# Performance work log

Measured on AMD Instinct MI355X. Metric: run time of the kernel, lower is better.

The kernel has to match this reference:

```python
import jax, jax.numpy as jnp
import numpy as np

D_IN = 784
D = 768          # hidden_dim
R = 8            # num_rels
L = 3            # num_layers
B = 64           # graphs in batch
N = 32768        # total nodes
E = 262144       # total edges


def _layer_norm(x, g, b, eps=1e-5):
    m = x.mean(-1, keepdims=True)
    v = x.var(-1, keepdims=True)
    return (x - m) / jnp.sqrt(v + eps) * g + b


def setup_inputs() -> dict:
    key = jax.random.key(0)
    ks = jax.random.split(key, 24)
    s = 0.02
    inp = {
        "type_vec": jax.random.normal(ks[0], (N, 16), jnp.float32),
        "code_vec": jax.random.normal(ks[1], (N, D), jnp.float32),
        # input_proj: Linear(784,768) + LayerNorm(768)
        "W_in": jax.random.normal(ks[2], (D_IN, D), jnp.float32) * s,
        "b_in": jnp.zeros((D,), jnp.float32),
        "ln_in_g": jnp.ones((D,), jnp.float32),
        "ln_in_b": jnp.zeros((D,), jnp.float32),
        # RGCN layers (basis regularizer, num_bases=num_rels -> per-relation W)
        "W_rel": jax.random.normal(ks[3], (L, R, D, D), jnp.float32) * s,
        "W_loop": jax.random.normal(ks[4], (L, D, D), jnp.float32) * s,
        "rgcn_bias": jnp.zeros((L, D), jnp.float32),
        "ln_g": jnp.ones((L, D), jnp.float32),
        "ln_b": jnp.zeros((L, D), jnp.float32),
        # global attention pooling gate MLP: 768 -> 384 -> 1
        "Wg1": jax.random.normal(ks[5], (D, D // 2), jnp.float32) * s,
        "bg1": jnp.zeros((D // 2,), jnp.float32),
        "Wg2": jax.random.normal(ks[6], (D // 2, 1), jnp.float32) * s,
        "bg2": jnp.zeros((1,), jnp.float32),
        # classifier: 768 -> 512 (+LN) -> 2
        "Wc1": jax.random.normal(ks[7], (D, 512), jnp.float32) * s,
        "bc1": jnp.zeros((512,), jnp.float32),
        "ln_c_g": jnp.ones((512,), jnp.float32),
        "ln_c_b": jnp.zeros((512,), jnp.float32),
        "Wc2": jax.random.normal(ks[8], (512, 2), jnp.float32) * s,
        "bc2": jnp.zeros((2,), jnp.float32),
        # graph structure
        "src": jax.random.randint(ks[9], (E,), 0, N, jnp.int64),
        "dst": jax.random.randint(ks[10], (E,), 0, N, jnp.int64),
        "edge_type": jax.random.randint(ks[11], (E,), 0, R, jnp.int64),
        "node_graph": jnp.sort(jax.random.randint(ks[12], (N,), 0, B, jnp.int64)),
        "num_graphs": B,
    }
    return inp


def reference(type_vec, code_vec, W_in, b_in, ln_in_g, ln_in_b,
              W_rel, W_loop, rgcn_bias, ln_g, ln_b,
              Wg1, bg1, Wg2, bg2, Wc1, bc1, ln_c_g, ln_c_b, Wc2, bc2,
              src, dst, edge_type, node_graph, num_graphs):
    # input projection
    h = jnp.concatenate([type_vec, code_vec], axis=-1)           # [N, 784]
    h = jax.nn.gelu(_layer_norm(h @ W_in + b_in, ln_in_g, ln_in_b), approximate=False)
    n_nodes = h.shape[0]
    n_layers, n_rels = W_rel.shape[0], W_rel.shape[1]

    for l in range(n_layers):
        agg = jnp.zeros_like(h)
        for r in range(n_rels):
            # relation-specific transform, then gather->mask->scatter-add
            msg = (h @ W_rel[l, r])[src] * (edge_type == r).astype(h.dtype)[:, None]  # [E, D]
            agg = agg + jax.ops.segment_sum(msg, dst, num_segments=n_nodes)
        h_new = agg + rgcn_bias[l] + h @ W_loop[l]               # DGL: agg + bias + self-loop
        h = jax.nn.gelu(_layer_norm(h_new, ln_g[l], ln_b[l]), approximate=False)

    # global attention pooling (segment softmax over nodes of each graph)
    gate = (jax.nn.gelu(h @ Wg1 + bg1, approximate=False) @ Wg2 + bg2)[:, 0]  # [N]
    gmax = jax.ops.segment_max(gate, node_graph, num_segments=num_graphs)
    e = jnp.exp(gate - gmax[node_graph])
    denom = jax.ops.segment_sum(e, node_graph, num_segments=num_graphs)
    w = e / denom[node_graph]
    graph_repr = jax.ops.segment_sum(w[:, None] * h, node_graph, num_segments=num_graphs)  # [B, D]

    # classifier head
    z = jax.nn.gelu(_layer_norm(graph_repr @ Wc1 + bc1, ln_c_g, ln_c_b), approximate=False)
    logits = z @ Wc2 + bc2
    return jax.nn.log_softmax(logits, axis=-1)
```

## Files before the change

kernel.cpp:

```cpp
#include <hip/hip_runtime.h>
#include <hip/hip_bf16.h>

typedef __hip_bfloat16 bf16;
typedef __attribute__((ext_vector_type(8))) __bf16 bf16x8;
typedef __attribute__((ext_vector_type(4))) float f32x4;

#define N_NODES 32768
#define N_EDGES 262144
#define DIM 768
#define NGR 64
#define KIN 800
#define KSTACK 6912
#define NKEY (N_NODES * 8)

#define GLOBAL_AS __attribute__((address_space(1)))
#define LDS_AS __attribute__((address_space(3)))

__device__ __forceinline__ float gelu_f(float x) {
    return 0.5f * x * (1.0f + erff(x * 0.70710678118654752f));
}
__device__ __forceinline__ float bfu(unsigned short v) {
    union { unsigned u; float f; } x; x.u = (unsigned)v << 16; return x.f;
}
__device__ __forceinline__ unsigned short fbf(float f) {
    bf16 t = __float2bfloat16(f); return *(unsigned short*)&t;
}

__global__ __launch_bounds__(256)
void tcast_k(const float* __restrict__ in, bf16* __restrict__ out, int I, int O,
             int Ipad, int ostride) {
    __shared__ float t[32][33];
    const int i0 = blockIdx.x * 32, o0 = blockIdx.y * 32;
    const int tx = threadIdx.x & 31, ty = threadIdx.x >> 5;
#pragma unroll
    for (int q = 0; q < 4; ++q) {
        int i = i0 + ty + q * 8, o = o0 + tx;
        t[ty + q * 8][tx] = (i < I) ? in[(size_t)i * O + o] : 0.0f;
    }
    __syncthreads();
#pragma unroll
    for (int q = 0; q < 4; ++q) {
        int o = o0 + ty + q * 8, i = i0 + tx;
        if (i < Ipad) out[(size_t)o * ostride + i] = __float2bfloat16(t[tx][ty + q * 8]);
    }
}

__global__ __launch_bounds__(256)
void wprep_l_k(const float* __restrict__ Wrel_l, const float* __restrict__ Wloop_l,
               bf16* __restrict__ WstL) {
    __shared__ float t[32][33];
    const int q = blockIdx.z;
    const float* in = (q < 8) ? Wrel_l + (size_t)q * DIM * DIM : Wloop_l;
    bf16* out = WstL + (q < 8 ? (q + 1) * DIM : 0);
    const int i0 = blockIdx.x * 32, o0 = blockIdx.y * 32;
    const int tx = threadIdx.x & 31, ty = threadIdx.x >> 5;
#pragma unroll
    for (int qq = 0; qq < 4; ++qq)
        t[ty + qq * 8][tx] = in[(size_t)(i0 + ty + qq * 8) * DIM + o0 + tx];
    __syncthreads();
#pragma unroll
    for (int qq = 0; qq < 4; ++qq)
        out[(size_t)(o0 + ty + qq * 8) * KSTACK + i0 + tx] =
            __float2bfloat16(t[tx][ty + qq * 8]);
}

__global__ __launch_bounds__(256)
void concat_k(const float* __restrict__ tv, const float* __restrict__ cv, bf16* __restrict__ X) {
    const int n = blockIdx.x;
    for (int c = threadIdx.x; c < KIN; c += 256) {
        float v = 0.0f;
        if (c < 16) v = tv[(size_t)n * 16 + c];
        else if (c < 784) v = cv[(size_t)n * DIM + (c - 16)];
        X[(size_t)n * KIN + c] = __float2bfloat16(v);
    }
}

__global__ __launch_bounds__(256)
void hist2_k(const int* __restrict__ dst, const int* __restrict__ et, int* __restrict__ cur) {
    int e = blockIdx.x * 256 + threadIdx.x;
    if (e < N_EDGES) atomicAdd(&cur[dst[e] * 8 + et[e]], 1);
}

__global__ __launch_bounds__(1024)
void scan2_k(int* __restrict__ cur, int* __restrict__ rp) {
    __shared__ int part[1024];
    const int t = threadIdx.x;
    const int base_i = t * 256;
    int s = 0;
    for (int i = 0; i < 256; ++i) s += cur[base_i + i];
    part[t] = s; __syncthreads();
    for (int st = 1; st < 1024; st <<= 1) {
        int v = (t >= st) ? part[t - st] : 0;
        __syncthreads();
        part[t] += v;
        __syncthreads();
    }
    int run = part[t] - s;
    for (int i = 0; i < 256; ++i) {
        int d = cur[base_i + i];
        rp[base_i + i] = run; cur[base_i + i] = run;
        run += d;
    }
    if (t == 1023) rp[NKEY] = run;
}

__global__ __launch_bounds__(256)
void place2_k(const int* __restrict__ src, const int* __restrict__ dst,
              const int* __restrict__ et, int* __restrict__ cur,
              int* __restrict__ eidx) {
    int e = blockIdx.x * 256 + threadIdx.x;
    if (e >= N_EDGES) return;
    int pos = atomicAdd(&cur[dst[e] * 8 + et[e]], 1);
    eidx[pos] = (et[e] << 16) | src[e];
}

template <int NC>
__global__ __launch_bounds__(256)
void gather8(const bf16* __restrict__ h, const int* __restrict__ rp2,
             const int* __restrict__ eidx, bf16* __restrict__ AGG,
             int rbase, int ostride, int colbase) {
    const int wave = threadIdx.x >> 6, lane = threadIdx.x & 63;
    const int n = blockIdx.x * 4 + wave;
    const int c0 = 4 * lane;
    unsigned short* outrow = (unsigned short*)&AGG[(size_t)n * ostride + colbase];
    const int* bp = &rp2[n * 8 + rbase];
    for (int sel = 0; sel < NC; ++sel) {
        const int s = bp[sel], e = bp[sel + 1];
        float f[12];
#pragma unroll
        for (int j = 0; j < 12; ++j) f[j] = 0.f;
        for (int t = s; t < e; ++t) {
            const int srcn = eidx[t] & 0xffff;
            const unsigned short* hs = (const unsigned short*)&h[(size_t)srcn * DIM];
#pragma unroll
            for (int j = 0; j < 3; ++j) {
                ushort4 u = *(const ushort4*)&hs[c0 + j * 256];
                f[4 * j + 0] += bfu(u.x); f[4 * j + 1] += bfu(u.y);
                f[4 * j + 2] += bfu(u.z); f[4 * j + 3] += bfu(u.w);
            }
        }
#pragma unroll
        for (int j = 0; j < 3; ++j) {
            ushort4 o;
            o.x = fbf(f[4 * j + 0]); o.y = fbf(f[4 * j + 1]);
            o.z = fbf(f[4 * j + 2]); o.w = fbf(f[4 * j + 3]);
            *(ushort4*)&outrow[sel * DIM + c0 + j * 256] = o;
        }
    }
}

template <int MODE>
__global__ __launch_bounds__(512, 2)
void gemm384(const bf16* __restrict__ A1, int S1, int K1,
             const bf16* __restrict__ A2, int S2,
             const bf16* __restrict__ BT, int ldb,
             bf16* __restrict__ OUT, int Nn, int Ktot, int nbx) {
    __shared__ __align__(16) unsigned short lA[3][256 * 32];
    __shared__ __align__(16) unsigned short lB[3][384 * 32];
    const int nblk = gridDim.x, qx = nblk >> 3, bid = blockIdx.x;
    const int wgid = (bid & 7) * qx + (bid >> 3);
    const int bx = wgid % nbx, by = wgid / nbx;
    const int bn = bx * 384, bm = by * 256;
    const int tid = threadIdx.x;
    const int wave = tid >> 6, lane = tid & 63;
    const int wr = wave >> 1, wc = wave & 1;
    const int l15 = lane & 15, lg = lane >> 4;
    const int swz = (lg ^ ((l15 >> 1) & 3)) * 8;

    f32x4 acc[4][12] = {};
    const int nkt = Ktot >> 5;

    auto stage = [&](int t, int buf) {
        const int k0 = t * 32;
        const bf16* Ab; int koff, stA;
        if (k0 < K1) { Ab = A1; koff = k0; stA = S1; }
        else         { Ab = A2; koff = k0 - K1; stA = S2; }
#pragma unroll
        for (int u = 0; u < 2; ++u) {
            const int c = u * 512 + tid;
            const int r = c >> 2, s = c & 3;
            const int sc = (s ^ ((r >> 1) & 3)) * 8;
            const bf16* ga = Ab + (size_t)(bm + r) * stA + koff + sc;
            __builtin_amdgcn_global_load_lds((const GLOBAL_AS void*)ga,
                (LDS_AS void*)&lA[buf][(u * 512 + wave * 64) * 8], 16, 0, 0);
        }
#pragma unroll
        for (int u = 0; u < 3; ++u) {
            const int c = u * 512 + tid;
            const int r = c >> 2, s = c & 3;
            const int sc = (s ^ ((r >> 1) & 3)) * 8;
            const bf16* gb = BT + (size_t)(bn + r) * ldb + k0 + sc;
            __builtin_amdgcn_global_load_lds((const GLOBAL_AS void*)gb,
                (LDS_AS void*)&lB[buf][(u * 512 + wave * 64) * 8], 16, 0, 0);
        }
    };

    stage(0, 0);
    if (nkt > 1) stage(1, 1);

    int rb = 0;
    for (int t = 0; t < nkt; ++t) {
        if (t + 2 < nkt) {
            int sb = rb + 2; if (sb >= 3) sb -= 3;
            stage(t + 2, sb);
            asm volatile("s_waitcnt vmcnt(10)" ::: "memory");
        } else if (t + 1 < nkt) {
            asm volatile("s_waitcnt vmcnt(5)" ::: "memory");
        } else {
            asm volatile("s_waitcnt vmcnt(0)" ::: "memory");
        }
        __builtin_amdgcn_s_barrier();
        __builtin_amdgcn_sched_barrier(0);

        bf16x8 af[4];
#pragma unroll
        for (int mi = 0; mi < 4; ++mi) {
            const int r = wr * 64 + mi * 16 + l15;
            af[mi] = *reinterpret_cast<const bf16x8*>(&lA[rb][r * 32 + swz]);
        }
        __builtin_amdgcn_s_setprio(1);
#pragma unroll
        for (int ni = 0; ni < 12; ++ni) {
            const int r = wc * 192 + ni * 16 + l15;
            bf16x8 bq = *reinterpret_cast<const bf16x8*>(&lB[rb][r * 32 + swz]);
#pragma unroll
            for (int mi = 0; mi < 4; ++mi)
                acc[mi][ni] = __builtin_amdgcn_mfma_f32_16x16x32_bf16(af[mi], bq, acc[mi][ni], 0, 0, 0);
        }
        __builtin_amdgcn_s_setprio(0);
        __builtin_amdgcn_sched_barrier(0);
        __builtin_amdgcn_s_barrier();

        rb = (rb == 2) ? 0 : rb + 1;
    }

    unsigned short* O = (unsigned short*)OUT;
#pragma unroll
    for (int mi = 0; mi < 4; ++mi)
#pragma unroll
        for (int ni = 0; ni < 12; ++ni) {
            const int r0 = bm + wr * 64 + mi * 16 + lg * 4;
            const int c0 = bn + wc * 192 + ni * 16 + l15;
#pragma unroll
            for (int i = 0; i < 4; ++i) {
                size_t idx = (size_t)(r0 + i) * Nn + c0;
                float v = acc[mi][ni][i];
                if (MODE == 1) v += bfu(O[idx]);
                O[idx] = fbf(v);
            }
        }
}

__global__ __launch_bounds__(256)
void ln_gelu_k(const bf16* __restrict__ ACCb, const float* __restrict__ bias,
               const float* __restrict__ g, const float* __restrict__ b,
               bf16* __restrict__ hout) {
    const int wave = threadIdx.x >> 6, lane = threadIdx.x & 63;
    const int n = blockIdx.x * 4 + wave;
    const unsigned short* Ab = (const unsigned short*)ACCb;
    float x[12];
    float s = 0.f, ss = 0.f;
#pragma unroll
    for (int j = 0; j < 12; ++j) {
        int c = lane + j * 64;
        x[j] = bfu(Ab[(size_t)n * DIM + c]) + bias[c];
        s += x[j]; ss += x[j] * x[j];
    }
#pragma unroll
    for (int m = 1; m < 64; m <<= 1) { s += __shfl_xor(s, m, 64); ss += __shfl_xor(ss, m, 64); }
    const float mean = s * (1.f / DIM);
    const float var = ss * (1.f / DIM) - mean * mean;
    const float rstd = rsqrtf(var + 1e-5f);
#pragma unroll
    for (int j = 0; j < 12; ++j) {
        int c = lane + j * 64;
        float y = (x[j] - mean) * rstd * g[c] + b[c];
        hout[(size_t)n * DIM + c] = __float2bfloat16(gelu_f(y));
    }
}

__global__ __launch_bounds__(256)
void gate_k(const bf16* __restrict__ G1, const float* __restrict__ bg1,
            const float* __restrict__ Wg2, const float* __restrict__ bg2,
            float* __restrict__ gate) {
    const int wave = threadIdx.x >> 6, lane = threadIdx.x & 63;
    const int n = blockIdx.x * 4 + wave;
    const unsigned short* G = (const unsigned short*)G1;
    float acc = 0.f;
#pragma unroll
    for (int j = 0; j < 6; ++j) {
        int c = lane + j * 64;
        float xv = bfu(G[(size_t)n * 384 + c]) + bg1[c];
        acc += gelu_f(xv) * Wg2[c];
    }
#pragma unroll
    for (int m = 1; m < 64; m <<= 1) acc += __shfl_xor(acc, m, 64);
    if (lane == 0) gate[n] = acc + bg2[0];
}

__device__ __forceinline__ int lower_bound_ng(const int* ng, int key) {
    int lo = 0, hi = N_NODES;
    while (lo < hi) { int mid = (lo + hi) >> 1; if (ng[mid] < key) lo = mid + 1; else hi = mid; }
    return lo;
}

__global__ __launch_bounds__(256)
void seg_stats_k(const float* __restrict__ gate, const int* __restrict__ ng,
                 float* __restrict__ gmax, float* __restrict__ gden) {
    __shared__ float red[256];
    const int b = blockIdx.x, t = threadIdx.x;
    const int start = lower_bound_ng(ng, b), end = lower_bound_ng(ng, b + 1);
    float m = -1e30f;
    for (int n = start + t; n < end; n += 256) m = fmaxf(m, gate[n]);
    red[t] = m; __syncthreads();
    for (int s = 128; s > 0; s >>= 1) { if (t < s) red[t] = fmaxf(red[t], red[t + s]); __syncthreads(); }
    const float gm = red[0]; __syncthreads();
    float ssum = 0.f;
    for (int n = start + t; n < end; n += 256) ssum += expf(gate[n] - gm);
    red[t] = ssum; __syncthreads();
    for (int s = 128; s > 0; s >>= 1) { if (t < s) red[t] += red[t + s]; __syncthreads(); }
    if (t == 0) { gmax[b] = gm; gden[b] = fmaxf(red[0], 1e-30f); }
}

__global__ __launch_bounds__(768)
void pool_k(const bf16* __restrict__ h, const float* __restrict__ gate,
            const int* __restrict__ ng, const float* __restrict__ gmax,
            const float* __restrict__ gden, float* __restrict__ grep) {
    const int b = blockIdx.x, c = threadIdx.x;
    const int start = lower_bound_ng(ng, b), end = lower_bound_ng(ng, b + 1);
    const float gm = gmax[b], inv = 1.0f / gden[b];
    const unsigned short* hv = (const unsigned short*)h;
    float a0 = 0.f, a1 = 0.f;
    int n = start;
    for (; n + 1 < end; n += 2) {
        float w0 = expf(gate[n] - gm) * inv;
        float w1 = expf(gate[n + 1] - gm) * inv;
        a0 += w0 * bfu(hv[(size_t)n * DIM + c]);
        a1 += w1 * bfu(hv[(size_t)(n + 1) * DIM + c]);
    }
    if (n < end) a0 += expf(gate[n] - gm) * inv * bfu(hv[(size_t)n * DIM + c]);
    grep[(size_t)b * DIM + c] = a0 + a1;
}

__global__ __launch_bounds__(512)
void cls_k(const float* __restrict__ grep, const float* __restrict__ Wc1,
           const float* __restrict__ bc1, const float* __restrict__ lng,
           const float* __restrict__ lnb, const float* __restrict__ Wc2,
           const float* __restrict__ bc2, float* __restrict__ out) {
    __shared__ float gr[DIM];
    __shared__ float red[512];
    const int b = blockIdx.x, j = threadIdx.x;
    for (int c = j; c < DIM; c += 512) gr[c] = grep[(size_t)b * DIM + c];
    __syncthreads();
    float a = bc1[j];
#pragma unroll 4
    for (int k = 0; k < DIM; ++k) a = fmaf(gr[k], Wc1[(size_t)k * 512 + j], a);
    red[j] = a; __syncthreads();
    for (int s = 256; s > 0; s >>= 1) { if (j < s) red[j] += red[j + s]; __syncthreads(); }
    const float mean = red[0] * (1.f / 512.f);
    __syncthreads();
    red[j] = (a - mean) * (a - mean); __syncthreads();
    for (int s = 256; s > 0; s >>= 1) { if (j < s) red[j] += red[j + s]; __syncthreads(); }
    const float rstd = rsqrtf(red[0] * (1.f / 512.f) + 1e-5f);
    __syncthreads();
    const float z = gelu_f((a - mean) * rstd * lng[j] + lnb[j]);
    red[j] = z * Wc2[2 * j + 0]; __syncthreads();
    for (int s = 256; s > 0; s >>= 1) { if (j < s) red[j] += red[j + s]; __syncthreads(); }
    const float l0 = red[0] + bc2[0];
    __syncthreads();
    red[j] = z * Wc2[2 * j + 1]; __syncthreads();
    for (int s = 256; s > 0; s >>= 1) { if (j < s) red[j] += red[j + s]; __syncthreads(); }
    if (j == 0) {
        const float l1 = red[0] + bc2[1];
        const float mx = fmaxf(l0, l1);
        const float lse = mx + logf(expf(l0 - mx) + expf(l1 - mx));
        out[2 * b + 0] = l0 - lse;
        out[2 * b + 1] = l1 - lse;
    }
}

extern "C" void kernel_launch(void* const* d_in, const int* in_sizes, int n_in,
                              void* d_out, int out_size, void* d_ws, size_t ws_size,
                              hipStream_t stream) {
    const float* type_vec = (const float*)d_in[0];
    const float* code_vec = (const float*)d_in[1];
    const float* W_in     = (const float*)d_in[2];
    const float* b_in     = (const float*)d_in[3];
    const float* ln_in_g  = (const float*)d_in[4];
    const float* ln_in_b  = (const float*)d_in[5];
    const float* W_rel    = (const float*)d_in[6];
    const float* W_loop   = (const float*)d_in[7];
    const float* rgcn_bias= (const float*)d_in[8];
    const float* ln_g     = (const float*)d_in[9];
    const float* ln_b     = (const float*)d_in[10];
    const float* Wg1      = (const float*)d_in[11];
    const float* bg1      = (const float*)d_in[12];
    const float* Wg2      = (const float*)d_in[13];
    const float* bg2      = (const float*)d_in[14];
    const float* Wc1      = (const float*)d_in[15];
    const float* bc1      = (const float*)d_in[16];
    const float* ln_c_g   = (const float*)d_in[17];
    const float* ln_c_b   = (const float*)d_in[18];
    const float* Wc2      = (const float*)d_in[19];
    const float* bc2      = (const float*)d_in[20];
    const int* src        = (const int*)d_in[21];
    const int* dst        = (const int*)d_in[22];
    const int* etype      = (const int*)d_in[23];
    const int* node_graph = (const int*)d_in[24];

    char* ws = (char*)d_ws;

    auto lay = [&](int nc, bool doAssign,
                   bf16*& h_bf, bf16*& ACCb, bf16*& WstL, int*& rp2, int*& cur2,
                   int*& eidx, float*& gate, float*& gmax, float*& gden,
                   float*& grep, bf16*& AGG) -> size_t {
        size_t off = 0;
        auto alloc = [&](size_t sz) { size_t r = off; off = (off + sz + 255) & ~(size_t)255; return r; };
        size_t oH   = alloc((size_t)N_NODES * DIM * 2);
        size_t oAC  = alloc((size_t)N_NODES * DIM * 2);
        size_t oWL  = alloc((size_t)DIM * KSTACK * 2);
        size_t oRP  = alloc((size_t)(NKEY + 1) * 4);
        size_t oCU  = alloc((size_t)NKEY * 4);
        size_t oEI  = alloc((size_t)N_EDGES * 4);
        size_t oGA  = alloc((size_t)N_NODES * 4);
        size_t oGM  = alloc(256);
        size_t oGD  = alloc(256);
        size_t oGR  = alloc((size_t)NGR * DIM * 4);
        size_t oAG  = alloc((size_t)N_NODES * nc * DIM * 2);
        if (doAssign) {
            h_bf = (bf16*)(ws + oH);   ACCb = (bf16*)(ws + oAC);
            WstL = (bf16*)(ws + oWL);  rp2  = (int*)(ws + oRP);
            cur2 = (int*)(ws + oCU);   eidx = (int*)(ws + oEI);
            gate = (float*)(ws + oGA); gmax = (float*)(ws + oGM);
            gden = (float*)(ws + oGD); grep = (float*)(ws + oGR);
            AGG  = (bf16*)(ws + oAG);
        }
        return off;
    };

    bf16 *h_bf, *ACCb, *WstL, *AGG; int *rp2, *cur2, *eidx;
    float *gate, *gmax, *gden, *grep;
    bf16 *d0=nullptr,*d1=nullptr,*d2=nullptr,*d3=nullptr; int *d4=nullptr,*d5=nullptr,*d6=nullptr;
    float *d7=nullptr,*d8=nullptr,*d9=nullptr,*d10=nullptr;
    const bool big = ws_size >= lay(8, false, d0,d1,d2,d4,d5,d6,d7,d8,d9,d10,d3);
    const int nc = big ? 8 : 4;
    lay(nc, true, h_bf, ACCb, WstL, rp2, cur2, eidx, gate, gmax, gden, grep, AGG);

    bf16* Xbf  = AGG;
    bf16* WinT = (bf16*)((char*)AGG + (size_t)N_NODES * KIN * 2);
    bf16* G1   = AGG;

    const int AGW = nc * DIM;

    tcast_k<<<dim3(25, 24), 256, 0, stream>>>(W_in, WinT, 784, DIM, KIN, KIN);
    concat_k<<<N_NODES, 256, 0, stream>>>(type_vec, code_vec, Xbf);
    gemm384<0><<<256, 512, 0, stream>>>(Xbf, KIN, KIN, Xbf, KIN, WinT, KIN, ACCb, DIM, KIN, 2);
    ln_gelu_k<<<N_NODES / 4, 256, 0, stream>>>(ACCb, b_in, ln_in_g, ln_in_b, h_bf);

    hipMemsetAsync(cur2, 0, (size_t)NKEY * 4, stream);
    hist2_k<<<N_EDGES / 256, 256, 0, stream>>>(dst, etype, cur2);
    scan2_k<<<1, 1024, 0, stream>>>(cur2, rp2);
    place2_k<<<N_EDGES / 256, 256, 0, stream>>>(src, dst, etype, cur2, eidx);

    for (int l = 0; l < 3; ++l) {
        wprep_l_k<<<dim3(24, 24, 9), 256, 0, stream>>>(
            W_rel + (size_t)l * 8 * DIM * DIM, W_loop + (size_t)l * DIM * DIM, WstL);
        if (nc == 8) {
            gather8<8><<<N_NODES / 4, 256, 0, stream>>>(h_bf, rp2, eidx, AGG, 0, AGW, 0);
            gemm384<0><<<256, 512, 0, stream>>>(
                h_bf, DIM, DIM, AGG, AGW, WstL, KSTACK, ACCb, DIM, KSTACK, 2);
        } else {
            gather8<4><<<N_NODES / 4, 256, 0, stream>>>(h_bf, rp2, eidx, AGG, 0, AGW, 0);
            gemm384<0><<<256, 512, 0, stream>>>(
                h_bf, DIM, DIM, AGG, AGW, WstL, KSTACK, ACCb, DIM, DIM + 4 * DIM, 2);
            gather8<4><<<N_NODES / 4, 256, 0, stream>>>(h_bf, rp2, eidx, AGG, 4, AGW, 0);
            gemm384<1><<<256, 512, 0, stream>>>(
                AGG, AGW, AGW, AGG, AGW, WstL + (size_t)DIM * 5, KSTACK, ACCb, DIM, 4 * DIM, 2);
        }
        ln_gelu_k<<<N_NODES / 4, 256, 0, stream>>>(ACCb, rgcn_bias + l * DIM, ln_g + l * DIM,
                                                   ln_b + l * DIM, h_bf);
    }

    bf16* Wg1T = (bf16*)((char*)AGG + 60 * 1024 * 1024);
    tcast_k<<<dim3(24, 12), 256, 0, stream>>>(Wg1, Wg1T, DIM, 384, DIM, DIM);
    gemm384<0><<<128, 512, 0, stream>>>(h_bf, DIM, DIM, h_bf, DIM, Wg1T, DIM, G1, 384, DIM, 1);
    gate_k<<<N_NODES / 4, 256, 0, stream>>>(G1, bg1, Wg2, bg2, gate);
    seg_stats_k<<<NGR, 256, 0, stream>>>(gate, node_graph, gmax, gden);
    pool_k<<<NGR, 768, 0, stream>>>(h_bf, gate, node_graph, gmax, gden, grep);

    cls_k<<<NGR, 512, 0, stream>>>(grep, Wc1, bc1, ln_c_g, ln_c_b, Wc2, bc2, (float*)d_out);
}
```

Baseline: 2.453 ms.

## Fuse LayerNorm+GELU into full-row GEMM epilogue and single-pass relation gather

Adds a GEMM kernel whose tiles span all 768 output columns. Bias, LayerNorm and GELU can then run in the epilogue, with row statistics reduced through shuffles and LDS. This removes the separate ln_gelu pass and the round trip of the fp32/bf16 accumulator buffer for the input projection and every RGCN layer. It also replaces the per-relation gather loop with one pass over each node's edges that accumulates into eight register sets chosen by relation. The cost is very high register pressure (4x12 MFMA accumulators plus 96 gather accumulators), which risks spills or lower occupancy.

```diff
diff --git a/kernel.cpp b/kernel.cpp
--- a/kernel.cpp
+++ b/kernel.cpp
@@ -114,6 +114,46 @@
     eidx[pos] = (et[e] << 16) | src[e];
 }
 
+__global__ __launch_bounds__(256)
+void gather1p(const bf16* __restrict__ h, const int* __restrict__ rp2,
+              const int* __restrict__ eidx, bf16* __restrict__ AGG, int ostride) {
+    const int wave = threadIdx.x >> 6, lane = threadIdx.x & 63;
+    const int n = blockIdx.x * 4 + wave;
+    const int c0 = 4 * lane;
+    const int start = rp2[n * 8], end = rp2[n * 8 + 8];
+    float f0[12] = {}, f1[12] = {}, f2[12] = {}, f3[12] = {};
+    float f4[12] = {}, f5[12] = {}, f6[12] = {}, f7[12] = {};
+    for (int t = start; t < end; ++t) {
+        const int pk = eidx[t];
+        const int sel = pk >> 16;
+        const unsigned short* hs = (const unsigned short*)&h[(size_t)(pk & 0xffff) * DIM];
+        ushort4 u0 = *(const ushort4*)&hs[c0];
+        ushort4 u1 = *(const ushort4*)&hs[c0 + 256];
+        ushort4 u2 = *(const ushort4*)&hs[c0 + 512];
+#define ADDE(F) { F[0]+=bfu(u0.x); F[1]+=bfu(u0.y); F[2]+=bfu(u0.z); F[3]+=bfu(u0.w); \
+                  F[4]+=bfu(u1.x); F[5]+=bfu(u1.y); F[6]+=bfu(u1.z); F[7]+=bfu(u1.w); \
+                  F[8]+=bfu(u2.x); F[9]+=bfu(u2.y); F[10]+=bfu(u2.z); F[11]+=bfu(u2.w); }
+        switch (sel) {
+            case 0: ADDE(f0) break;
+            case 1: ADDE(f1) break;
+            case 2: ADDE(f2) break;
+            case 3: ADDE(f3) break;
+            case 4: ADDE(f4) break;
+            case 5: ADDE(f5) break;
+            case 6: ADDE(f6) break;
+            default: ADDE(f7) break;
+        }
+#undef ADDE
+    }
+    unsigned short* outrow = (unsigned short*)&AGG[(size_t)n * ostride];
+#define STE(F, S) _Pragma("unroll") for (int j = 0; j < 3; ++j) { ushort4 o; \
+        o.x = fbf(F[4*j+0]); o.y = fbf(F[4*j+1]); o.z = fbf(F[4*j+2]); o.w = fbf(F[4*j+3]); \
+        *(ushort4*)&outrow[(S) * DIM + c0 + j * 256] = o; }
+    STE(f0, 0) STE(f1, 1) STE(f2, 2) STE(f3, 3)
+    STE(f4, 4) STE(f5, 5) STE(f6, 6) STE(f7, 7)
+#undef STE
+}
+
 template <int NC>
 __global__ __launch_bounds__(256)
 void gather8(const bf16* __restrict__ h, const int* __restrict__ rp2,
@@ -147,6 +187,137 @@
             *(ushort4*)&outrow[sel * DIM + c0 + j * 256] = o;
         }
     }
+}
+
+__global__ __launch_bounds__(512, 2)
+void gemm_ln(const bf16* __restrict__ A1, int S1, int K1,
+             const bf16* __restrict__ A2, int S2,
+             const bf16* __restrict__ BT, int ldb,
+             const float* __restrict__ bias, const float* __restrict__ g,
+             const float* __restrict__ b, bf16* __restrict__ OUT, int Ktot) {
+    __shared__ __align__(16) unsigned short lA[2][128 * 32];
+    __shared__ __align__(16) unsigned short lB[2][768 * 32];
+    __shared__ float lred[128][8];
+    const int nblk = gridDim.x, qx = nblk >> 3, bid = blockIdx.x;
+    const int wgid = (bid & 7) * qx + (bid >> 3);
+    const int bm = wgid * 128;
+    const int tid = threadIdx.x;
+    const int wave = tid >> 6, lane = tid & 63;
+    const int wr = wave >> 2, wc = wave & 3;
+    const int l15 = lane & 15, lg = lane >> 4;
+    const int swz = (lg ^ ((l15 >> 1) & 3)) * 8;
+
+    f32x4 acc[4][12] = {};
+    const int nkt = Ktot >> 5;
+
+    auto stage = [&](int t, int buf) {
+        const int k0 = t * 32;
+        const bf16* Ab; int koff, stA;
+        if (k0 < K1) { Ab = A1; koff = k0; stA = S1; }
+        else         { Ab = A2; koff = k0 - K1; stA = S2; }
+        {
+            const int r = tid >> 2, s = tid & 3;
+            const int sc = (s ^ ((r >> 1) & 3)) * 8;
+            const bf16* ga = Ab + (size_t)(bm + r) * stA + koff + sc;
+            __builtin_amdgcn_global_load_lds((const GLOBAL_AS void*)ga,
+                (LDS_AS void*)&lA[buf][(wave * 64) * 8], 16, 0, 0);
+        }
+#pragma unroll
+        for (int u = 0; u < 6; ++u) {
+            const int c = u * 512 + tid;
+            const int r = c >> 2, s = c & 3;
+            const int sc = (s ^ ((r >> 1) & 3)) * 8;
+            const bf16* gb = BT + (size_t)r * ldb + k0 + sc;
+            __builtin_amdgcn_global_load_lds((const GLOBAL_AS void*)gb,
+                (LDS_AS void*)&lB[buf][((u * 8 + wave) * 64) * 8], 16, 0, 0);
+        }
+    };
+
+    stage(0, 0);
+
+    for (int t = 0; t < nkt; ++t) {
+        const int rb = t & 1;
+        if (t + 1 < nkt) {
+            stage(t + 1, rb ^ 1);
+            asm volatile("s_waitcnt vmcnt(7)" ::: "memory");
+        } else {
+            asm volatile("s_waitcnt vmcnt(0)" ::: "memory");
+        }
+        __builtin_amdgcn_s_barrier();
+        __builtin_amdgcn_sched_barrier(0);
+
+        bf16x8 af[4];
+#pragma unroll
+        for (int mi = 0; mi < 4; ++mi) {
+            const int r = wr * 64 + mi * 16 + l15;
+            af[mi] = *reinterpret_cast<const bf16x8*>(&lA[rb][r * 32 + swz]);
+        }
+        __builtin_amdgcn_s_setprio(1);
+#pragma unroll
+        for (int ni = 0; ni < 12; ++ni) {
+            const int r = wc * 192 + ni * 16 + l15;
+            bf16x8 bq = *reinterpret_cast<const bf16x8*>(&lB[rb][r * 32 + swz]);
+#pragma unroll
+            for (int mi = 0; mi < 4; ++mi)
+                acc[mi][ni] = __builtin_amdgcn_mfma_f32_16x16x32_bf16(af[mi], bq, acc[mi][ni], 0, 0, 0);
+        }
+        __builtin_amdgcn_s_setprio(0);
+        __builtin_amdgcn_sched_barrier(0);
+        __builtin_amdgcn_s_barrier();
+    }
+
+    float biasv[12], gv[12], bvv[12];
+#pragma unroll
+    for (int ni = 0; ni < 12; ++ni) {
+        const int col = wc * 192 + ni * 16 + l15;
+        biasv[ni] = bias[col]; gv[ni] = g[col]; bvv[ni] = b[col];
+    }
+#pragma unroll
+    for (int mi = 0; mi < 4; ++mi)
+#pragma unroll
+        for (int ni = 0; ni < 12; ++ni)
+#pragma unroll
+            for (int i = 0; i < 4; ++i)
+                acc[mi][ni][i] += biasv[ni];
+#pragma unroll
+    for (int mi = 0; mi < 4; ++mi)
+#pragma unroll
+        for (int i = 0; i < 4; ++i) {
+            float s = 0.f, ss = 0.f;
+#pragma unroll
+            for (int ni = 0; ni < 12; ++ni) {
+                float v = acc[mi][ni][i];
+                s += v; ss += v * v;
+            }
+#pragma unroll
+            for (int m = 1; m < 16; m <<= 1) {
+                s += __shfl_xor(s, m, 64); ss += __shfl_xor(ss, m, 64);
+            }
+            if (l15 == 0) {
+                const int rloc = wr * 64 + mi * 16 + lg * 4 + i;
+                lred[rloc][wc] = s; lred[rloc][4 + wc] = ss;
+            }
+        }
+    __syncthreads();
+    unsigned short* O = (unsigned short*)OUT;
+#pragma unroll
+    for (int mi = 0; mi < 4; ++mi)
+#pragma unroll
+        for (int i = 0; i < 4; ++i) {
+            const int rloc = wr * 64 + mi * 16 + lg * 4 + i;
+            const float s = lred[rloc][0] + lred[rloc][1] + lred[rloc][2] + lred[rloc][3];
+            const float q = lred[rloc][4] + lred[rloc][5] + lred[rloc][6] + lred[rloc][7];
+            const float mean = s * (1.f / DIM);
+            const float var = q * (1.f / DIM) - mean * mean;
+            const float rstd = rsqrtf(var + 1e-5f);
+            const size_t rowoff = (size_t)(bm + rloc) * DIM;
+#pragma unroll
+            for (int ni = 0; ni < 12; ++ni) {
+                const int col = wc * 192 + ni * 16 + l15;
+                const float y = (acc[mi][ni][i] - mean) * rstd * gv[ni] + bvv[ni];
+                O[rowoff + col] = fbf(gelu_f(y));
+            }
+        }
 }
 
 template <int MODE>
@@ -454,8 +625,13 @@
 
     tcast_k<<<dim3(25, 24), 256, 0, stream>>>(W_in, WinT, 784, DIM, KIN, KIN);
     concat_k<<<N_NODES, 256, 0, stream>>>(type_vec, code_vec, Xbf);
-    gemm384<0><<<256, 512, 0, stream>>>(Xbf, KIN, KIN, Xbf, KIN, WinT, KIN, ACCb, DIM, KIN, 2);
-    ln_gelu_k<<<N_NODES / 4, 256, 0, stream>>>(ACCb, b_in, ln_in_g, ln_in_b, h_bf);
+    if (big) {
+        gemm_ln<<<256, 512, 0, stream>>>(Xbf, KIN, KIN, Xbf, KIN, WinT, KIN,
+                                         b_in, ln_in_g, ln_in_b, h_bf, KIN);
+    } else {
+        gemm384<0><<<256, 512, 0, stream>>>(Xbf, KIN, KIN, Xbf, KIN, WinT, KIN, ACCb, DIM, KIN, 2);
+        ln_gelu_k<<<N_NODES / 4, 256, 0, stream>>>(ACCb, b_in, ln_in_g, ln_in_b, h_bf);
+    }
 
     hipMemsetAsync(cur2, 0, (size_t)NKEY * 4, stream);
     hist2_k<<<N_EDGES / 256, 256, 0, stream>>>(dst, etype, cur2);
@@ -466,9 +642,10 @@
         wprep_l_k<<<dim3(24, 24, 9), 256, 0, stream>>>(
             W_rel + (size_t)l * 8 * DIM * DIM, W_loop + (size_t)l * DIM * DIM, WstL);
         if (nc == 8) {
-            gather8<8><<<N_NODES / 4, 256, 0, stream>>>(h_bf, rp2, eidx, AGG, 0, AGW, 0);
-            gemm384<0><<<256, 512, 0, stream>>>(
-                h_bf, DIM, DIM, AGG, AGW, WstL, KSTACK, ACCb, DIM, KSTACK, 2);
+            gather1p<<<N_NODES / 4, 256, 0, stream>>>(h_bf, rp2, eidx, AGG, AGW);
+            gemm_ln<<<256, 512, 0, stream>>>(h_bf, DIM, DIM, AGG, AGW, WstL, KSTACK,
+                                             rgcn_bias + l * DIM, ln_g + l * DIM,
+                                             ln_b + l * DIM, h_bf, KSTACK);
         } else {
             gather8<4><<<N_NODES / 4, 256, 0, stream>>>(h_bf, rp2, eidx, AGG, 0, AGW, 0);
             gemm384<0><<<256, 512, 0, stream>>>(
@@ -476,9 +653,9 @@
             gather8<4><<<N_NODES / 4, 256, 0, stream>>>(h_bf, rp2, eidx, AGG, 4, AGW, 0);
             gemm384<1><<<256, 512, 0, stream>>>(
                 AGG, AGW, AGW, AGG, AGW, WstL + (size_t)DIM * 5, KSTACK, ACCb, DIM, 4 * DIM, 2);
-        }
-        ln_gelu_k<<<N_NODES / 4, 256, 0, stream>>>(ACCb, rgcn_bias + l * DIM, ln_g + l * DIM,
-                                                   ln_b + l * DIM, h_bf);
+            ln_gelu_k<<<N_NODES / 4, 256, 0, stream>>>(ACCb, rgcn_bias + l * DIM, ln_g + l * DIM,
+                                                       ln_b + l * DIM, h_bf);
+        }
     }
 
     bf16* Wg1T = (bf16*)((char*)AGG + 60 * 1024 * 1024);
```

After: 2.446 ms. No clear change (-0.3%).
